# Kernel tuning notes

Hardware: AMD Instinct MI355X
Metric: run time of the kernel (lower is better)

The kernel has to match this reference:

```python
import jax, jax.numpy as jnp
import numpy as np

NUM_GROUPS = 32
EPS = 1e-6


def group_norm(x, gamma, beta):
    # x: [B, C, H, W]
    B, C, H, W = x.shape
    xg = x.reshape(B, NUM_GROUPS, C // NUM_GROUPS, H, W)
    mean = jnp.mean(xg, axis=(2, 3, 4), keepdims=True)
    var = jnp.var(xg, axis=(2, 3, 4), keepdims=True)
    xn = ((xg - mean) * jax.lax.rsqrt(var + EPS)).reshape(B, C, H, W)
    return xn * gamma[None, :, None, None] + beta[None, :, None, None]


def conv1x1(x, w, b):
    # x: [B, C, H, W], w: [O, C], b: [O]  (1x1 conv == channel matmul)
    return jnp.einsum('oc,bchw->bohw', w, x) + b[None, :, None, None]


def setup_inputs() -> dict:
    key = jax.random.key(0)
    ks = jax.random.split(key, 10)
    B, C, H, W = 16, 512, 32, 32
    s = 1.0 / np.sqrt(C)
    inp = {
        'hidden_states': jax.random.normal(ks[0], (B, C, H, W), dtype=jnp.float32),
        'norm_gamma': jnp.ones((C,), dtype=jnp.float32),
        'norm_beta': jnp.zeros((C,), dtype=jnp.float32),
        'wq': jax.random.normal(ks[1], (C, C), dtype=jnp.float32) * s,
        'bq': jnp.zeros((C,), dtype=jnp.float32),
        'wk': jax.random.normal(ks[2], (C, C), dtype=jnp.float32) * s,
        'bk': jnp.zeros((C,), dtype=jnp.float32),
        'wv': jax.random.normal(ks[3], (C, C), dtype=jnp.float32) * s,
        'bv': jnp.zeros((C,), dtype=jnp.float32),
        'wo': jax.random.normal(ks[4], (C, C), dtype=jnp.float32) * s,
        'bo': jnp.zeros((C,), dtype=jnp.float32),
    }
    return inp


def reference(hidden_states, norm_gamma, norm_beta, wq, bq, wk, bk, wv, bv, wo, bo):
    residual = hidden_states
    h = group_norm(hidden_states, norm_gamma, norm_beta)
    q = conv1x1(h, wq, bq)  # [B, C, H, W]
    k = conv1x1(h, wk, bk)
    v = conv1x1(h, wv, bv)
    B, C, H, W = q.shape
    N = H * W
    qf = q.reshape(B, C, N)  # [B, C, N]
    kf = k.reshape(B, C, N)
    vf = v.reshape(B, C, N)
    scale = float(C) ** (-0.5)
    # attn_weights[b, i, j] = sum_c q[b,c,i] * k[b,c,j]
    attn = jnp.einsum('bci,bcj->bij', qf, kf) * scale
    attn = jax.nn.softmax(attn, axis=2)
    # out[b, c, i] = sum_j v[b,c,j] * attn[b,i,j]
    out = jnp.einsum('bcj,bij->bci', vf, attn).reshape(B, C, H, W)
    out = conv1x1(out, wo, bo)
    return residual + out
```

## Files before the change

### kernel.cpp

```cpp
#include <hip/hip_runtime.h>

typedef __attribute__((ext_vector_type(4))) float f32x4;
typedef __attribute__((ext_vector_type(8))) __bf16 bf16x8;
typedef __attribute__((ext_vector_type(4))) unsigned short us4;
typedef __attribute__((ext_vector_type(8))) unsigned short us8;

#define B_  16
#define C_  512
#define N_  1024
#define G_  32
#define GS  16

__device__ inline unsigned short f2bf(float f) {
  unsigned u = __builtin_bit_cast(unsigned, f);
  u += 0x7fffu + ((u >> 16) & 1u);
  return (unsigned short)(u >> 16);
}

#define GLOAD_LDS16(gp, lp) __builtin_amdgcn_global_load_lds( \
    (const __attribute__((address_space(1))) unsigned int*)(gp), \
    (__attribute__((address_space(3))) unsigned int*)(lp), 16, 0, 0)

__global__ __launch_bounds__(256) void gn_stats(const float* __restrict__ x,
                                                float* __restrict__ stats) {
  int bg = blockIdx.x;
  const float* xp = x + (long)bg * (GS * N_);
  int tid = threadIdx.x;
  float s = 0.f, ss = 0.f;
  for (int i = tid * 4; i < GS * N_; i += 1024) {
    f32x4 v = *(const f32x4*)&xp[i];
    s += v.x + v.y + v.z + v.w;
    ss += v.x * v.x + v.y * v.y + v.z * v.z + v.w * v.w;
  }
  __shared__ float r1[256], r2[256];
  r1[tid] = s; r2[tid] = ss; __syncthreads();
  for (int off = 128; off > 0; off >>= 1) {
    if (tid < off) { r1[tid] += r1[tid + off]; r2[tid] += r2[tid + off]; }
    __syncthreads();
  }
  if (tid == 0) {
    float mean = r1[0] * (1.f / (GS * N_));
    float var  = r2[0] * (1.f / (GS * N_)) - mean * mean;
    stats[bg * 2]     = mean;
    stats[bg * 2 + 1] = rsqrtf(var + 1e-6f);
  }
}

__global__ __launch_bounds__(256) void gn_apply(const float* __restrict__ x,
                                                const float* __restrict__ stats,
                                                const float* __restrict__ gamma,
                                                const float* __restrict__ beta,
                                                unsigned short* __restrict__ ht) {
  int b = blockIdx.z, ct = blockIdx.y, nt = blockIdx.x;
  int c0 = ct * 64, n0 = nt * 64;
  int tid = threadIdx.x;
  __shared__ unsigned short L[64 * 68];
  const float* xp = x + ((long)b * C_ + c0) * N_ + n0;
#pragma unroll
  for (int i = 0; i < 4; ++i) {
    int li = tid + i * 256;
    int row = li >> 4;
    int col4 = (li & 15) * 4;
    f32x4 v = *(const f32x4*)&xp[(long)row * N_ + col4];
    int c = c0 + row;
    float mean = stats[(b * G_ + (c >> 4)) * 2];
    float rstd = stats[(b * G_ + (c >> 4)) * 2 + 1];
    float gm = gamma[c] * rstd;
    float bt = beta[c] - mean * gm;
    us4 o;
    o.x = f2bf(v.x * gm + bt); o.y = f2bf(v.y * gm + bt);
    o.z = f2bf(v.z * gm + bt); o.w = f2bf(v.w * gm + bt);
    *(us4*)&L[row * 68 + col4] = o;
  }
  __syncthreads();
#pragma unroll
  for (int i = 0; i < 2; ++i) {
    int s = tid + i * 256;
    int n = s >> 3;
    int cs = (s & 7) * 8;
    us8 o;
#pragma unroll
    for (int j = 0; j < 8; ++j) o[j] = L[(cs + j) * 68 + n];
    *(us8*)&ht[((long)b * N_ + n0 + n) * C_ + c0 + cs] = o;
  }
}

__global__ __launch_bounds__(256) void convert_w(const float* __restrict__ wq, const float* __restrict__ wk,
                                                 const float* __restrict__ wv, const float* __restrict__ wo,
                                                 const float* __restrict__ bq, const float* __restrict__ bk,
                                                 unsigned short* __restrict__ wqk, unsigned short* __restrict__ wvb,
                                                 unsigned short* __restrict__ wob, float* __restrict__ bqk) {
  int i = blockIdx.x * 256 + threadIdx.x;
  if (i < C_ * C_) {
    wqk[i]           = f2bf(wq[i]);
    wqk[C_ * C_ + i] = f2bf(wk[i]);
    wvb[i]           = f2bf(wv[i]);
    wob[i]           = f2bf(wo[i]);
  }
  if (i < C_) { bqk[i] = bq[i]; bqk[C_ + i] = bk[i]; }
}

__device__ inline f32x4 mfma16(bf16x8 a, bf16x8 b, f32x4 c) {
  return __builtin_amdgcn_mfma_f32_16x16x32_bf16(a, b, c, 0, 0, 0);
}

__device__ inline int swz(int b) { return b ^ (((b >> 9) & 1) << 5); }

template<int NREP, int EPI>
__global__ __launch_bounds__(512, 2) void gemm256(
    const unsigned short* __restrict__ A, long lda, long Az,
    const unsigned short* __restrict__ Bm, long ldb, long Bz,
    void* __restrict__ Dp, long ldd, long Dz,
    const float* __restrict__ bias, float scale, int K,
    const float* __restrict__ residual, float* __restrict__ rs) {
  constexpr int BN = NREP * 64;
  const int z = blockIdx.z;
  const long row0 = (long)blockIdx.x * 256;
  const long col0 = (long)blockIdx.y * BN;
  const int tid  = threadIdx.x;
  const int lane = tid & 63;
  const int wave = tid >> 6;
  const int wm = wave >> 2;
  const int wn = wave & 3;
  const int lr = lane & 15;
  const int khb = (lane >> 4) * 16;

  __shared__ unsigned short Abuf[2][16384];
  __shared__ unsigned short Bbuf[2][BN * 64];
  __shared__ float dinv_s[256];

  const unsigned short* Ab = A  + (long)z * Az;
  const unsigned short* Bb = Bm + (long)z * Bz;

  if constexpr (EPI == 6) {
    if (tid < 256) {
      const float* rp = rs + ((long)z * 1024 + row0 + tid) * 16;
      float s = 0.f;
#pragma unroll
      for (int i = 0; i < 16; ++i) s += rp[i];
      dinv_s[tid] = 1.f / s;
    }
    asm volatile("s_waitcnt lgkmcnt(0)" ::: "memory");
  }

  const unsigned short* gA[4];
#pragma unroll
  for (int r = 0; r < 4; ++r) {
    int L = swz(r * 8192 + tid * 16);
    gA[r] = Ab + (row0 + (L >> 7)) * lda + ((L & 127) >> 1);
  }
  const unsigned short* gB[NREP];
#pragma unroll
  for (int r = 0; r < NREP; ++r) {
    int L = swz(r * 8192 + tid * 16);
    gB[r] = Bb + (col0 + (L >> 7)) * ldb + ((L & 127) >> 1);
  }

  f32x4 acc[8][NREP];
#pragma unroll
  for (int m = 0; m < 8; ++m)
#pragma unroll
    for (int n = 0; n < NREP; ++n) acc[m][n] = f32x4{0.f, 0.f, 0.f, 0.f};

  const int NT = K >> 6;
#pragma unroll
  for (int r = 0; r < 4; ++r)    GLOAD_LDS16(gA[r], &Abuf[0][r * 4096 + wave * 512]);
#pragma unroll
  for (int r = 0; r < NREP; ++r) GLOAD_LDS16(gB[r], &Bbuf[0][r * 4096 + wave * 512]);

  for (int t = 0; t < NT; ++t) {
    int tn = t + 1; if (tn == NT) tn = 0;
    const long ko = (long)tn << 6;
    const int nb = (t + 1) & 1;
#pragma unroll
    for (int r = 0; r < 4; ++r)    GLOAD_LDS16(gA[r] + ko, &Abuf[nb][r * 4096 + wave * 512]);
#pragma unroll
    for (int r = 0; r < NREP; ++r) GLOAD_LDS16(gB[r] + ko, &Bbuf[nb][r * 4096 + wave * 512]);
    if constexpr (NREP == 4) asm volatile("s_waitcnt vmcnt(8)" ::: "memory");
    else                     asm volatile("s_waitcnt vmcnt(6)" ::: "memory");
    __builtin_amdgcn_s_barrier();
    __builtin_amdgcn_sched_barrier(0);
    const unsigned short* Al = Abuf[t & 1];
    const unsigned short* Bl = Bbuf[t & 1];
#pragma unroll
    for (int kk = 0; kk < 2; ++kk) {
      bf16x8 af[8], bfr[NREP];
#pragma unroll
      for (int m = 0; m < 8; ++m) {
        int Pb = swz((wm * 128 + m * 16 + lr) * 128 + kk * 64 + khb);
        af[m] = *(const bf16x8*)((const char*)Al + Pb);
      }
#pragma unroll
      for (int n = 0; n < NREP; ++n) {
        int Pb = swz((wn * NREP * 16 + n * 16 + lr) * 128 + kk * 64 + khb);
        bfr[n] = *(const bf16x8*)((const char*)Bl + Pb);
      }
      __builtin_amdgcn_s_setprio(1);
#pragma unroll
      for (int m = 0; m < 8; ++m)
#pragma unroll
        for (int n = 0; n < NREP; ++n)
          acc[m][n] = mfma16(af[m], bfr[n], acc[m][n]);
      __builtin_amdgcn_s_setprio(0);
    }
    __builtin_amdgcn_sched_barrier(0);
    __builtin_amdgcn_s_barrier();
    __builtin_amdgcn_sched_barrier(0);
  }
  asm volatile("s_waitcnt vmcnt(0)" ::: "memory");

  const int rb = (lane >> 4) * 4;
  if constexpr (EPI == 5) {
    const int jt = blockIdx.y;
#pragma unroll
    for (int m = 0; m < 8; ++m) {
      float ps[4] = {0.f, 0.f, 0.f, 0.f};
#pragma unroll
      for (int n = 0; n < NREP; ++n) {
#pragma unroll
        for (int r = 0; r < 4; ++r) {
          long gr = row0 + wm * 128 + m * 16 + rb + r;
          long gc = col0 + wn * NREP * 16 + n * 16 + lr;
          float e = exp2f(acc[m][n][r] * scale);
          ((unsigned short*)Dp)[(long)z * Dz + gr * ldd + gc] = f2bf(e);
          ps[r] += e;
        }
      }
#pragma unroll
      for (int r = 0; r < 4; ++r) {
        ps[r] += __shfl_xor(ps[r], 1);
        ps[r] += __shfl_xor(ps[r], 2);
        ps[r] += __shfl_xor(ps[r], 4);
        ps[r] += __shfl_xor(ps[r], 8);
      }
      if (lr == 0) {
#pragma unroll
        for (int r = 0; r < 4; ++r) {
          long gr = row0 + wm * 128 + m * 16 + rb + r;
          rs[((long)z * 1024 + gr) * 16 + jt * 4 + wn] = ps[r];
        }
      }
    }
    return;
  }

#pragma unroll
  for (int m = 0; m < 8; ++m) {
#pragma unroll
    for (int n = 0; n < NREP; ++n) {
#pragma unroll
      for (int r = 0; r < 4; ++r) {
        long gr = row0 + wm * 128 + m * 16 + rb + r;
        long gc = col0 + wn * NREP * 16 + n * 16 + lr;
        float v = acc[m][n][r];
        if constexpr (EPI == 0) {
          v += bias[gc];
          ((unsigned short*)Dp)[(long)z * Dz + gr * ldd + gc] = f2bf(v);
        } else if constexpr (EPI == 1) {
          v += bias[gr];
          ((unsigned short*)Dp)[(long)z * Dz + gr * ldd + gc] = f2bf(v);
        } else if constexpr (EPI == 6) {
          v *= dinv_s[(int)(wm * 128 + m * 16 + rb + r)];
          ((unsigned short*)Dp)[(long)z * Dz + gr * ldd + gc] = f2bf(v);
        } else {
          long o = (long)z * (512L * 1024L) + gr * 1024L + gc;
          ((float*)Dp)[o] = v + bias[gr] + residual[o];
        }
      }
    }
  }
}

extern "C" void kernel_launch(void* const* d_in, const int* in_sizes, int n_in,
                              void* d_out, int out_size, void* d_ws, size_t ws_size,
                              hipStream_t stream) {
  const float* x     = (const float*)d_in[0];
  const float* gamma = (const float*)d_in[1];
  const float* beta  = (const float*)d_in[2];
  const float* wq    = (const float*)d_in[3];
  const float* bq    = (const float*)d_in[4];
  const float* wk    = (const float*)d_in[5];
  const float* bk    = (const float*)d_in[6];
  const float* wv    = (const float*)d_in[7];
  const float* bv    = (const float*)d_in[8];
  const float* wo    = (const float*)d_in[9];
  const float* bo    = (const float*)d_in[10];
  float* out = (float*)d_out;

  char* ws = (char*)d_ws;
  unsigned short* ht   = (unsigned short*)(ws + 0);
  unsigned short* qkt  = (unsigned short*)(ws + 16777216);
  unsigned short* vv   = (unsigned short*)(ws + 50331648);
  unsigned short* ot   = (unsigned short*)(ws + 67108864);
  unsigned short* S    = (unsigned short*)(ws + 83886080);
  unsigned short* wqkb = (unsigned short*)(ws + 117440512);
  unsigned short* wvb  = (unsigned short*)(ws + 119537664);
  unsigned short* wob  = (unsigned short*)(ws + 120061952);
  float* bqk           = (float*)(ws + 120586240);
  float* stats         = (float*)(ws + 120590336);
  float* rs            = (float*)(ws + 120594432);

  convert_w<<<1024, 256, 0, stream>>>(wq, wk, wv, wo, bq, bk, wqkb, wvb, wob, bqk);
  gn_stats<<<512, 256, 0, stream>>>(x, stats);
  gn_apply<<<dim3(16, 8, 16), 256, 0, stream>>>(x, stats, gamma, beta, ht);

  gemm256<4, 0><<<dim3(64, 4, 1), 512, 0, stream>>>(ht, 512, 0, wqkb, 512, 0,
                                                    qkt, 1024, 0, bqk, 0.f, 512, nullptr, nullptr);
  gemm256<2, 1><<<dim3(2, 128, 1), 512, 0, stream>>>(wvb, 512, 0, ht, 512, 0,
                                                     vv, 16384, 0, bv, 0.f, 512, nullptr, nullptr);
  gemm256<4, 5><<<dim3(4, 4, 16), 512, 0, stream>>>(qkt, 1024, 1048576L, qkt + 512, 1024, 1048576L,
                                                    S, 1024, 1048576L, nullptr,
                                                    0.06375871416f, 512, nullptr, rs);
  gemm256<2, 6><<<dim3(4, 4, 16), 512, 0, stream>>>(S, 1024, 1048576L,
                                                    vv, 16384, 1024,
                                                    ot, 512, 524288L, nullptr, 0.f, 1024, nullptr, rs);
  gemm256<2, 4><<<dim3(2, 8, 16), 512, 0, stream>>>(wob, 512, 0, ot, 512, 524288L,
                                                    out, 0, 0, bo, 0.f, 512, x, nullptr);
}
```

Before: 152.8 us.

## Fuse weight conversion into GN stats and interleave GEMM loads with MFMA phases

Folds the bf16 weight conversion into the group-norm statistics kernel, which removes one kernel launch. It also restructures the GEMM main loop into several phases. Each phase issues part of the next tile's global-to-LDS loads, reads a sub-block of fragments, and runs a subset of MFMAs, with barriers between phases. This is meant to overlap memory traffic with matrix math and cut register pressure from fragments, at the cost of more barriers and a fragile vmcnt accounting.

```diff
diff --git a/kernel.cpp b/kernel.cpp
--- a/kernel.cpp
+++ b/kernel.cpp
@@ -21,11 +21,35 @@
     (const __attribute__((address_space(1))) unsigned int*)(gp), \
     (__attribute__((address_space(3))) unsigned int*)(lp), 16, 0, 0)
 
-__global__ __launch_bounds__(256) void gn_stats(const float* __restrict__ x,
-                                                float* __restrict__ stats) {
+__global__ __launch_bounds__(256) void gn_statsW(const float* __restrict__ x,
+                                                 float* __restrict__ stats,
+                                                 const float* __restrict__ wq, const float* __restrict__ wk,
+                                                 const float* __restrict__ wv, const float* __restrict__ wo,
+                                                 const float* __restrict__ bq, const float* __restrict__ bk,
+                                                 unsigned short* __restrict__ wqk, unsigned short* __restrict__ wvb,
+                                                 unsigned short* __restrict__ wob, float* __restrict__ bqk) {
   int bg = blockIdx.x;
+  int tid = threadIdx.x;
+  {
+    int base = bg * 512;
+#pragma unroll
+    for (int it = 0; it < 2; ++it) {
+      int i = base + it * 256 + tid;
+      wqk[i]           = f2bf(wq[i]);
+      wqk[262144 + i]  = f2bf(wk[i]);
+      wvb[i]           = f2bf(wv[i]);
+      wob[i]           = f2bf(wo[i]);
+    }
+    if (bg == 0) {
+#pragma unroll
+      for (int it = 0; it < 2; ++it) {
+        int j = it * 256 + tid;
+        bqk[j]       = bq[j];
+        bqk[512 + j] = bk[j];
+      }
+    }
+  }
   const float* xp = x + (long)bg * (GS * N_);
-  int tid = threadIdx.x;
   float s = 0.f, ss = 0.f;
   for (int i = tid * 4; i < GS * N_; i += 1024) {
     f32x4 v = *(const f32x4*)&xp[i];
@@ -83,21 +107,6 @@
     for (int j = 0; j < 8; ++j) o[j] = L[(cs + j) * 68 + n];
     *(us8*)&ht[((long)b * N_ + n0 + n) * C_ + c0 + cs] = o;
   }
-}
-
-__global__ __launch_bounds__(256) void convert_w(const float* __restrict__ wq, const float* __restrict__ wk,
-                                                 const float* __restrict__ wv, const float* __restrict__ wo,
-                                                 const float* __restrict__ bq, const float* __restrict__ bk,
-                                                 unsigned short* __restrict__ wqk, unsigned short* __restrict__ wvb,
-                                                 unsigned short* __restrict__ wob, float* __restrict__ bqk) {
-  int i = blockIdx.x * 256 + threadIdx.x;
-  if (i < C_ * C_) {
-    wqk[i]           = f2bf(wq[i]);
-    wqk[C_ * C_ + i] = f2bf(wk[i]);
-    wvb[i]           = f2bf(wv[i]);
-    wob[i]           = f2bf(wo[i]);
-  }
-  if (i < C_) { bqk[i] = bq[i]; bqk[C_ + i] = bk[i]; }
 }
 
 __device__ inline f32x4 mfma16(bf16x8 a, bf16x8 b, f32x4 c) {
@@ -126,7 +135,7 @@
   const int khb = (lane >> 4) * 16;
 
   __shared__ unsigned short Abuf[2][16384];
-  __shared__ unsigned short Bbuf[2][BN * 64];
+  __shared__ unsigned short Bbuf[2][NREP * 4096];
   __shared__ float dinv_s[256];
 
   const unsigned short* Ab = A  + (long)z * Az;
@@ -163,49 +172,140 @@
     for (int n = 0; n < NREP; ++n) acc[m][n] = f32x4{0.f, 0.f, 0.f, 0.f};
 
   const int NT = K >> 6;
-#pragma unroll
-  for (int r = 0; r < 4; ++r)    GLOAD_LDS16(gA[r], &Abuf[0][r * 4096 + wave * 512]);
-#pragma unroll
-  for (int r = 0; r < NREP; ++r) GLOAD_LDS16(gB[r], &Bbuf[0][r * 4096 + wave * 512]);
+  const int ldsO = wave * 512;
+
+  GLOAD_LDS16(gA[0], &Abuf[0][0     + ldsO]);
+  GLOAD_LDS16(gA[2], &Abuf[0][8192  + ldsO]);
+  GLOAD_LDS16(gA[1], &Abuf[0][4096  + ldsO]);
+  GLOAD_LDS16(gA[3], &Abuf[0][12288 + ldsO]);
+#pragma unroll
+  for (int r = 0; r < NREP; ++r) GLOAD_LDS16(gB[r], &Bbuf[0][r * 4096 + ldsO]);
+  GLOAD_LDS16(gA[0] + 64, &Abuf[1][0    + ldsO]);
+  GLOAD_LDS16(gA[2] + 64, &Abuf[1][8192 + ldsO]);
 
   for (int t = 0; t < NT; ++t) {
-    int tn = t + 1; if (tn == NT) tn = 0;
-    const long ko = (long)tn << 6;
-    const int nb = (t + 1) & 1;
-#pragma unroll
-    for (int r = 0; r < 4; ++r)    GLOAD_LDS16(gA[r] + ko, &Abuf[nb][r * 4096 + wave * 512]);
-#pragma unroll
-    for (int r = 0; r < NREP; ++r) GLOAD_LDS16(gB[r] + ko, &Bbuf[nb][r * 4096 + wave * 512]);
-    if constexpr (NREP == 4) asm volatile("s_waitcnt vmcnt(8)" ::: "memory");
-    else                     asm volatile("s_waitcnt vmcnt(6)" ::: "memory");
+    const int cur = t & 1, nxt = cur ^ 1;
+    int t1 = t + 1; if (t1 == NT) t1 = 0;
+    int t2 = t + 2; if (t2 >= NT) t2 -= NT;
+    const int ko1 = t1 << 6, ko2 = t2 << 6;
+    const unsigned short* Al = Abuf[cur];
+    const unsigned short* Bl = Bbuf[cur];
+    bf16x8 af[4][2];
+    bf16x8 bfr[NREP == 4 ? 4 : 2][2];
+
+    GLOAD_LDS16(gA[1] + ko1, &Abuf[nxt][4096  + ldsO]);
+    GLOAD_LDS16(gA[3] + ko1, &Abuf[nxt][12288 + ldsO]);
+    asm volatile("s_waitcnt vmcnt(4)" ::: "memory");
     __builtin_amdgcn_s_barrier();
     __builtin_amdgcn_sched_barrier(0);
-    const unsigned short* Al = Abuf[t & 1];
-    const unsigned short* Bl = Bbuf[t & 1];
 #pragma unroll
     for (int kk = 0; kk < 2; ++kk) {
-      bf16x8 af[8], bfr[NREP];
-#pragma unroll
-      for (int m = 0; m < 8; ++m) {
-        int Pb = swz((wm * 128 + m * 16 + lr) * 128 + kk * 64 + khb);
-        af[m] = *(const bf16x8*)((const char*)Al + Pb);
-      }
-#pragma unroll
-      for (int n = 0; n < NREP; ++n) {
-        int Pb = swz((wn * NREP * 16 + n * 16 + lr) * 128 + kk * 64 + khb);
-        bfr[n] = *(const bf16x8*)((const char*)Bl + Pb);
-      }
-      __builtin_amdgcn_s_setprio(1);
-#pragma unroll
-      for (int m = 0; m < 8; ++m)
-#pragma unroll
-        for (int n = 0; n < NREP; ++n)
-          acc[m][n] = mfma16(af[m], bfr[n], acc[m][n]);
-      __builtin_amdgcn_s_setprio(0);
-    }
+#pragma unroll
+      for (int n = 0; n < 2; ++n)
+        bfr[n][kk] = *(const bf16x8*)((const char*)Bl +
+                       swz((wn * (NREP * 16) + n * 16 + lr) * 128 + kk * 64 + khb));
+#pragma unroll
+      for (int m = 0; m < 4; ++m)
+        af[m][kk] = *(const bf16x8*)((const char*)Al +
+                       swz((wm * 128 + m * 16 + lr) * 128 + kk * 64 + khb));
+    }
+    __builtin_amdgcn_s_setprio(1);
+#pragma unroll
+    for (int kk = 0; kk < 2; ++kk)
+#pragma unroll
+      for (int m = 0; m < 4; ++m)
+#pragma unroll
+        for (int n = 0; n < 2; ++n)
+          acc[m][n] = mfma16(af[m][kk], bfr[n][kk], acc[m][n]);
+    __builtin_amdgcn_s_setprio(0);
     __builtin_amdgcn_sched_barrier(0);
     __builtin_amdgcn_s_barrier();
-    __builtin_amdgcn_sched_barrier(0);
+
+    if constexpr (NREP == 4) {
+      GLOAD_LDS16(gB[0] + ko1, &Bbuf[nxt][0    + ldsO]);
+      GLOAD_LDS16(gB[1] + ko1, &Bbuf[nxt][4096 + ldsO]);
+#pragma unroll
+      for (int kk = 0; kk < 2; ++kk)
+#pragma unroll
+        for (int n = 2; n < 4; ++n)
+          bfr[n][kk] = *(const bf16x8*)((const char*)Bl +
+                         swz((wn * 64 + n * 16 + lr) * 128 + kk * 64 + khb));
+      __builtin_amdgcn_s_barrier();
+      __builtin_amdgcn_sched_barrier(0);
+      __builtin_amdgcn_s_setprio(1);
+#pragma unroll
+      for (int kk = 0; kk < 2; ++kk)
+#pragma unroll
+        for (int m = 0; m < 4; ++m)
+#pragma unroll
+          for (int n = 2; n < 4; ++n)
+            acc[m][n] = mfma16(af[m][kk], bfr[n][kk], acc[m][n]);
+      __builtin_amdgcn_s_setprio(0);
+      __builtin_amdgcn_sched_barrier(0);
+      __builtin_amdgcn_s_barrier();
+
+      GLOAD_LDS16(gB[2] + ko1, &Bbuf[nxt][8192  + ldsO]);
+      GLOAD_LDS16(gB[3] + ko1, &Bbuf[nxt][12288 + ldsO]);
+#pragma unroll
+      for (int kk = 0; kk < 2; ++kk)
+#pragma unroll
+        for (int m = 0; m < 4; ++m)
+          af[m][kk] = *(const bf16x8*)((const char*)Al +
+                        swz((wm * 128 + 64 + m * 16 + lr) * 128 + kk * 64 + khb));
+      __builtin_amdgcn_s_barrier();
+      __builtin_amdgcn_sched_barrier(0);
+      __builtin_amdgcn_s_setprio(1);
+#pragma unroll
+      for (int kk = 0; kk < 2; ++kk)
+#pragma unroll
+        for (int m = 0; m < 4; ++m)
+#pragma unroll
+          for (int n = 0; n < 2; ++n)
+            acc[4 + m][n] = mfma16(af[m][kk], bfr[n][kk], acc[4 + m][n]);
+      __builtin_amdgcn_s_setprio(0);
+      __builtin_amdgcn_sched_barrier(0);
+      __builtin_amdgcn_s_barrier();
+
+      GLOAD_LDS16(gA[0] + ko2, &Abuf[cur][0    + ldsO]);
+      GLOAD_LDS16(gA[2] + ko2, &Abuf[cur][8192 + ldsO]);
+      __builtin_amdgcn_s_barrier();
+      __builtin_amdgcn_sched_barrier(0);
+      __builtin_amdgcn_s_setprio(1);
+#pragma unroll
+      for (int kk = 0; kk < 2; ++kk)
+#pragma unroll
+        for (int m = 0; m < 4; ++m)
+#pragma unroll
+          for (int n = 2; n < 4; ++n)
+            acc[4 + m][n] = mfma16(af[m][kk], bfr[n][kk], acc[4 + m][n]);
+      __builtin_amdgcn_s_setprio(0);
+      __builtin_amdgcn_sched_barrier(0);
+      __builtin_amdgcn_s_barrier();
+    } else {
+      GLOAD_LDS16(gB[0] + ko1, &Bbuf[nxt][0    + ldsO]);
+      GLOAD_LDS16(gB[1] + ko1, &Bbuf[nxt][4096 + ldsO]);
+      GLOAD_LDS16(gA[0] + ko2, &Abuf[cur][0    + ldsO]);
+      GLOAD_LDS16(gA[2] + ko2, &Abuf[cur][8192 + ldsO]);
+#pragma unroll
+      for (int kk = 0; kk < 2; ++kk)
+#pragma unroll
+        for (int m = 0; m < 4; ++m)
+          af[m][kk] = *(const bf16x8*)((const char*)Al +
+                        swz((wm * 128 + 64 + m * 16 + lr) * 128 + kk * 64 + khb));
+      __builtin_amdgcn_s_barrier();
+      __builtin_amdgcn_sched_barrier(0);
+      __builtin_amdgcn_s_setprio(1);
+#pragma unroll
+      for (int kk = 0; kk < 2; ++kk)
+#pragma unroll
+        for (int m = 0; m < 4; ++m)
+#pragma unroll
+          for (int n = 0; n < 2; ++n)
+            acc[4 + m][n] = mfma16(af[m][kk], bfr[n][kk], acc[4 + m][n]);
+      __builtin_amdgcn_s_setprio(0);
+      __builtin_amdgcn_sched_barrier(0);
+      __builtin_amdgcn_s_barrier();
+    }
   }
   asm volatile("s_waitcnt vmcnt(0)" ::: "memory");
 
@@ -300,8 +400,8 @@
   float* stats         = (float*)(ws + 120590336);
   float* rs            = (float*)(ws + 120594432);
 
-  convert_w<<<1024, 256, 0, stream>>>(wq, wk, wv, wo, bq, bk, wqkb, wvb, wob, bqk);
-  gn_stats<<<512, 256, 0, stream>>>(x, stats);
+  gn_statsW<<<512, 256, 0, stream>>>(x, stats, wq, wk, wv, wo, bq, bk,
+                                     wqkb, wvb, wob, bqk);
   gn_apply<<<dim3(16, 8, 16), 256, 0, stream>>>(x, stats, gamma, beta, ht);
 
   gemm256<4, 0><<<dim3(64, 4, 1), 512, 0, stream>>>(ht, 512, 0, wqkb, 512, 0,
```

New measurement: 167.3 us. +9.5%, slower.

## Fold output projection into value projection and fuse epilogue into PV GEMM

Applied to the files above, without the earlier changes.

Precomputes Wo·Wv (and Wo·bv) on device so the value projection directly produces Wo-projected values. The separate output-projection GEMM is removed and the PV GEMM epilogue applies softmax normalization, bias and residual, writing fp32 output. This drops one full 512x512x16K GEMM and an intermediate buffer round trip, at the cost of small weight-prep kernels and an extra bf16 rounding of the combined weight. Also adds a block-index swizzle for the attention GEMMs to improve cache locality.

```diff
diff --git a/kernel.cpp b/kernel.cpp
--- a/kernel.cpp
+++ b/kernel.cpp
@@ -86,27 +86,93 @@
 }
 
 __global__ __launch_bounds__(256) void convert_w(const float* __restrict__ wq, const float* __restrict__ wk,
-                                                 const float* __restrict__ wv, const float* __restrict__ wo,
+                                                 const float* __restrict__ wo,
                                                  const float* __restrict__ bq, const float* __restrict__ bk,
-                                                 unsigned short* __restrict__ wqk, unsigned short* __restrict__ wvb,
-                                                 unsigned short* __restrict__ wob, float* __restrict__ bqk) {
-  int i = blockIdx.x * 256 + threadIdx.x;
+                                                 const float* __restrict__ bv,
+                                                 unsigned short* __restrict__ wqk,
+                                                 unsigned short* __restrict__ wob, float* __restrict__ bqk,
+                                                 float* __restrict__ bvo) {
+  long bid = blockIdx.x;
+  int tid = threadIdx.x;
+  long i = bid * 256 + tid;
   if (i < C_ * C_) {
     wqk[i]           = f2bf(wq[i]);
     wqk[C_ * C_ + i] = f2bf(wk[i]);
-    wvb[i]           = f2bf(wv[i]);
     wob[i]           = f2bf(wo[i]);
   }
   if (i < C_) { bqk[i] = bq[i]; bqk[C_ + i] = bk[i]; }
+  if (bid >= 1024) {
+    int o = (int)(bid - 1024) * 256 + tid;
+    const float* wr = wo + (long)o * 512;
+    float acc = 0.f;
+    for (int c = 0; c < 512; c += 4) {
+      f32x4 w4 = *(const f32x4*)&wr[c];
+      f32x4 b4 = *(const f32x4*)&bv[c];
+      acc += w4.x * b4.x + w4.y * b4.y + w4.z * b4.z + w4.w * b4.w;
+    }
+    bvo[o] = acc;
+  }
+}
+
+__global__ __launch_bounds__(256) void transpose_wv(const float* __restrict__ wv,
+                                                    unsigned short* __restrict__ wvT) {
+  int c0 = blockIdx.x * 64, k0 = blockIdx.y * 64;
+  int tid = threadIdx.x;
+  __shared__ float Lt[64][65];
+#pragma unroll
+  for (int i = 0; i < 4; ++i) {
+    int lin = tid + i * 256;
+    int rr = lin >> 4;
+    int q4 = (lin & 15) * 4;
+    f32x4 v = *(const f32x4*)&wv[(long)(c0 + rr) * 512 + k0 + q4];
+    Lt[q4 + 0][rr] = v.x; Lt[q4 + 1][rr] = v.y;
+    Lt[q4 + 2][rr] = v.z; Lt[q4 + 3][rr] = v.w;
+  }
+  __syncthreads();
+#pragma unroll
+  for (int i = 0; i < 2; ++i) {
+    int lin = tid + i * 256;
+    int kk = lin >> 3;
+    int cc = (lin & 7) * 8;
+    us8 o;
+#pragma unroll
+    for (int j = 0; j < 8; ++j) o[j] = f2bf(Lt[kk][cc + j]);
+    *(us8*)&wvT[(long)(k0 + kk) * 512 + c0 + cc] = o;
+  }
 }
 
 __device__ inline f32x4 mfma16(bf16x8 a, bf16x8 b, f32x4 c) {
   return __builtin_amdgcn_mfma_f32_16x16x32_bf16(a, b, c, 0, 0, 0);
 }
 
+__global__ __launch_bounds__(256) void wprod(const unsigned short* __restrict__ wob,
+                                             const unsigned short* __restrict__ wvT,
+                                             unsigned short* __restrict__ WVO) {
+  int row0 = blockIdx.x * 64, col0 = blockIdx.y * 64;
+  int tid = threadIdx.x, lane = tid & 63, w = tid >> 6;
+  int lr = lane & 15, kh = (lane >> 4) * 8;
+  f32x4 acc4[4];
+#pragma unroll
+  for (int n = 0; n < 4; ++n) acc4[n] = f32x4{0.f, 0.f, 0.f, 0.f};
+  for (int k0 = 0; k0 < 512; k0 += 32) {
+    bf16x8 af = *(const bf16x8*)&wob[(long)(row0 + w * 16 + lr) * 512 + k0 + kh];
+#pragma unroll
+    for (int n = 0; n < 4; ++n) {
+      bf16x8 bf8 = *(const bf16x8*)&wvT[(long)(col0 + n * 16 + lr) * 512 + k0 + kh];
+      acc4[n] = mfma16(af, bf8, acc4[n]);
+    }
+  }
+  int rb = (lane >> 4) * 4;
+#pragma unroll
+  for (int n = 0; n < 4; ++n)
+#pragma unroll
+    for (int r = 0; r < 4; ++r)
+      WVO[(long)(row0 + w * 16 + rb + r) * 512 + col0 + n * 16 + lr] = f2bf(acc4[n][r]);
+}
+
 __device__ inline int swz(int b) { return b ^ (((b >> 9) & 1) << 5); }
 
-template<int NREP, int EPI>
+template<int NREP, int EPI, int XSWZ>
 __global__ __launch_bounds__(512, 2) void gemm256(
     const unsigned short* __restrict__ A, long lda, long Az,
     const unsigned short* __restrict__ Bm, long ldb, long Bz,
@@ -114,9 +180,15 @@
     const float* __restrict__ bias, float scale, int K,
     const float* __restrict__ residual, float* __restrict__ rs) {
   constexpr int BN = NREP * 64;
-  const int z = blockIdx.z;
-  const long row0 = (long)blockIdx.x * 256;
-  const long col0 = (long)blockIdx.y * BN;
+  int bx = blockIdx.x, by = blockIdx.y, bz = blockIdx.z;
+  if constexpr (XSWZ) {
+    int lin = bx + 4 * (by + 4 * bz);
+    int l2  = (lin & 7) * 32 + (lin >> 3);
+    bx = l2 & 3; by = (l2 >> 2) & 3; bz = l2 >> 4;
+  }
+  const int z = bz;
+  const long row0 = (long)bx * 256;
+  const long col0 = (long)by * BN;
   const int tid  = threadIdx.x;
   const int lane = tid & 63;
   const int wave = tid >> 6;
@@ -126,19 +198,19 @@
   const int khb = (lane >> 4) * 16;
 
   __shared__ unsigned short Abuf[2][16384];
-  __shared__ unsigned short Bbuf[2][BN * 64];
-  __shared__ float dinv_s[256];
+  __shared__ unsigned short Bbuf[2][NREP * 4096];
+  __shared__ float sred[256];
 
   const unsigned short* Ab = A  + (long)z * Az;
   const unsigned short* Bb = Bm + (long)z * Bz;
 
-  if constexpr (EPI == 6) {
+  if constexpr (EPI == 7) {
     if (tid < 256) {
       const float* rp = rs + ((long)z * 1024 + row0 + tid) * 16;
       float s = 0.f;
 #pragma unroll
       for (int i = 0; i < 16; ++i) s += rp[i];
-      dinv_s[tid] = 1.f / s;
+      sred[tid] = 1.f / s;
     }
     asm volatile("s_waitcnt lgkmcnt(0)" ::: "memory");
   }
@@ -192,7 +264,7 @@
       }
 #pragma unroll
       for (int n = 0; n < NREP; ++n) {
-        int Pb = swz((wn * NREP * 16 + n * 16 + lr) * 128 + kk * 64 + khb);
+        int Pb = swz((wn * (NREP * 16) + n * 16 + lr) * 128 + kk * 64 + khb);
         bfr[n] = *(const bf16x8*)((const char*)Bl + Pb);
       }
       __builtin_amdgcn_s_setprio(1);
@@ -211,7 +283,7 @@
 
   const int rb = (lane >> 4) * 4;
   if constexpr (EPI == 5) {
-    const int jt = blockIdx.y;
+    const int jt = by;
 #pragma unroll
     for (int m = 0; m < 8; ++m) {
       float ps[4] = {0.f, 0.f, 0.f, 0.f};
@@ -220,7 +292,7 @@
 #pragma unroll
         for (int r = 0; r < 4; ++r) {
           long gr = row0 + wm * 128 + m * 16 + rb + r;
-          long gc = col0 + wn * NREP * 16 + n * 16 + lr;
+          long gc = col0 + wn * (NREP * 16) + n * 16 + lr;
           float e = exp2f(acc[m][n][r] * scale);
           ((unsigned short*)Dp)[(long)z * Dz + gr * ldd + gc] = f2bf(e);
           ps[r] += e;
@@ -244,6 +316,27 @@
     return;
   }
 
+  if constexpr (EPI == 7) {
+#pragma unroll
+    for (int m = 0; m < 8; ++m) {
+      int lrow = wm * 128 + m * 16 + rb;
+      long gr0 = row0 + lrow;
+#pragma unroll
+      for (int n = 0; n < NREP; ++n) {
+        long gc = col0 + wn * (NREP * 16) + n * 16 + lr;
+        long o = (long)z * (512L * 1024L) + gc * 1024L + gr0;
+        f32x4 res = *(const f32x4*)&residual[o];
+        float bb = bias[gc];
+        f32x4 st;
+#pragma unroll
+        for (int r = 0; r < 4; ++r)
+          st[r] = acc[m][n][r] * sred[lrow + r] + bb + res[r];
+        *(f32x4*)&((float*)Dp)[o] = st;
+      }
+    }
+    return;
+  }
+
 #pragma unroll
   for (int m = 0; m < 8; ++m) {
 #pragma unroll
@@ -251,21 +344,11 @@
 #pragma unroll
       for (int r = 0; r < 4; ++r) {
         long gr = row0 + wm * 128 + m * 16 + rb + r;
-        long gc = col0 + wn * NREP * 16 + n * 16 + lr;
+        long gc = col0 + wn * (NREP * 16) + n * 16 + lr;
         float v = acc[m][n][r];
-        if constexpr (EPI == 0) {
-          v += bias[gc];
-          ((unsigned short*)Dp)[(long)z * Dz + gr * ldd + gc] = f2bf(v);
-        } else if constexpr (EPI == 1) {
-          v += bias[gr];
-          ((unsigned short*)Dp)[(long)z * Dz + gr * ldd + gc] = f2bf(v);
-        } else if constexpr (EPI == 6) {
-          v *= dinv_s[(int)(wm * 128 + m * 16 + rb + r)];
-          ((unsigned short*)Dp)[(long)z * Dz + gr * ldd + gc] = f2bf(v);
-        } else {
-          long o = (long)z * (512L * 1024L) + gr * 1024L + gc;
-          ((float*)Dp)[o] = v + bias[gr] + residual[o];
-        }
+        if constexpr (EPI == 0) v += bias[gc];
+        else                    v += bias[gr];
+        ((unsigned short*)Dp)[(long)z * Dz + gr * ldd + gc] = f2bf(v);
       }
     }
   }
@@ -290,30 +373,32 @@
   char* ws = (char*)d_ws;
   unsigned short* ht   = (unsigned short*)(ws + 0);
   unsigned short* qkt  = (unsigned short*)(ws + 16777216);
-  unsigned short* vv   = (unsigned short*)(ws + 50331648);
-  unsigned short* ot   = (unsigned short*)(ws + 67108864);
+  unsigned short* VWT  = (unsigned short*)(ws + 50331648);
   unsigned short* S    = (unsigned short*)(ws + 83886080);
   unsigned short* wqkb = (unsigned short*)(ws + 117440512);
-  unsigned short* wvb  = (unsigned short*)(ws + 119537664);
+  unsigned short* wvT  = (unsigned short*)(ws + 119537664);
   unsigned short* wob  = (unsigned short*)(ws + 120061952);
-  float* bqk           = (float*)(ws + 120586240);
-  float* stats         = (float*)(ws + 120590336);
-  float* rs            = (float*)(ws + 120594432);
-
-  convert_w<<<1024, 256, 0, stream>>>(wq, wk, wv, wo, bq, bk, wqkb, wvb, wob, bqk);
+  unsigned short* WVO  = (unsigned short*)(ws + 120586240);
+  float* bqk           = (float*)(ws + 121110528);
+  float* bvo           = (float*)(ws + 121114624);
+  float* stats         = (float*)(ws + 121116672);
+  float* rs            = (float*)(ws + 121122816);
+
+  convert_w<<<1026, 256, 0, stream>>>(wq, wk, wo, bq, bk, bv,
+                                      wqkb, wob, bqk, bvo);
+  transpose_wv<<<dim3(8, 8), 256, 0, stream>>>(wv, wvT);
+  wprod<<<dim3(8, 8), 256, 0, stream>>>(wob, wvT, WVO);
   gn_stats<<<512, 256, 0, stream>>>(x, stats);
   gn_apply<<<dim3(16, 8, 16), 256, 0, stream>>>(x, stats, gamma, beta, ht);
 
-  gemm256<4, 0><<<dim3(64, 4, 1), 512, 0, stream>>>(ht, 512, 0, wqkb, 512, 0,
-                                                    qkt, 1024, 0, bqk, 0.f, 512, nullptr, nullptr);
-  gemm256<2, 1><<<dim3(2, 128, 1), 512, 0, stream>>>(wvb, 512, 0, ht, 512, 0,
-                                                     vv, 16384, 0, bv, 0.f, 512, nullptr, nullptr);
-  gemm256<4, 5><<<dim3(4, 4, 16), 512, 0, stream>>>(qkt, 1024, 1048576L, qkt + 512, 1024, 1048576L,
-                                                    S, 1024, 1048576L, nullptr,
-                                                    0.06375871416f, 512, nullptr, rs);
-  gemm256<2, 6><<<dim3(4, 4, 16), 512, 0, stream>>>(S, 1024, 1048576L,
-                                                    vv, 16384, 1024,
-                                                    ot, 512, 524288L, nullptr, 0.f, 1024, nullptr, rs);
-  gemm256<2, 4><<<dim3(2, 8, 16), 512, 0, stream>>>(wob, 512, 0, ot, 512, 524288L,
-                                                    out, 0, 0, bo, 0.f, 512, x, nullptr);
-}
+  gemm256<4, 0, 0><<<dim3(64, 4, 1), 512, 0, stream>>>(ht, 512, 0, wqkb, 512, 0,
+                                                       qkt, 1024, 0, bqk, 0.f, 512, nullptr, nullptr);
+  gemm256<2, 1, 0><<<dim3(2, 128, 1), 512, 0, stream>>>(WVO, 512, 0, ht, 512, 0,
+                                                        VWT, 16384, 0, bvo, 0.f, 512, nullptr, nullptr);
+  gemm256<4, 5, 1><<<dim3(4, 4, 16), 512, 0, stream>>>(qkt, 1024, 1048576L, qkt + 512, 1024, 1048576L,
+                                                       S, 1024, 1048576L, nullptr,
+                                                       0.06375871416f, 512, nullptr, rs);
+  gemm256<2, 7, 1><<<dim3(4, 4, 16), 512, 0, stream>>>(S, 1024, 1048576L,
+                                                       VWT, 16384, 1024,
+                                                       out, 0, 0, bo, 0.f, 1024, x, rs);
+}
```

Result: no change. 155.3 us (+1.6%).
